# Kernel tuning notes

Hardware: AMD Instinct MI355X
Metric: run time of the kernel (lower is better)

The kernel has to match this reference:

```python
import jax, jax.numpy as jnp
import numpy as np

EMBED_DIM = 1024
FFN_DIM = 12  # == n_qubits; MeasureAll output dim must equal ffn_dim
BATCH, SEQ = 8, 2048


def setup_inputs() -> dict:
    key = jax.random.key(0)
    ks = jax.random.split(key, 6)
    s1 = 1.0 / np.sqrt(EMBED_DIM)
    s2 = 1.0 / np.sqrt(FFN_DIM)
    return {
        "x": jax.random.normal(ks[0], (BATCH, SEQ, EMBED_DIM), dtype=jnp.float32),
        "W1": jax.random.normal(ks[1], (FFN_DIM, EMBED_DIM), dtype=jnp.float32) * s1,
        "b1": jax.random.normal(ks[2], (FFN_DIM,), dtype=jnp.float32) * s1,
        "theta": jax.random.normal(ks[3], (FFN_DIM,), dtype=jnp.float32),
        "W2": jax.random.normal(ks[4], (EMBED_DIM, FFN_DIM), dtype=jnp.float32) * s2,
        "b2": jax.random.normal(ks[5], (EMBED_DIM,), dtype=jnp.float32) * s2,
    }


def reference(x, W1, b1, theta, W2, b2):
    # linear1 + ReLU: (B,S,E) -> (B,S,F)
    h = jax.nn.relu(jnp.einsum("bse,fe->bsf", x, W1) + b1)
    # QLayer: each wire i starts in |0>, gets RX(h_i) then RX(theta_i);
    # product state => <Z_i> = cos(h_i + theta_i) exactly (RX = exp(-i*phi*X/2)).
    q = jnp.cos(h + theta)
    # linear2 (dropout is identity in eval mode)
    return jnp.einsum("bsf,ef->bse", q, W2) + b2
```

## Files before the change

### kernel.cpp

```cpp
#include <hip/hip_runtime.h>
#include <hip/hip_bf16.h>

#define E 1024
#define F 12
#define BM 16

typedef float f32x4_t __attribute__((ext_vector_type(4)));
typedef short bf16x8  __attribute__((ext_vector_type(8)));

__device__ __forceinline__ short f2bf(float f) {
    return (short)__builtin_bit_cast(unsigned short, __float2bfloat16(f));
}

__global__ __launch_bounds__(256, 4) void ffq_mfma(
    const float* __restrict__ x,
    const float* __restrict__ W1,
    const float* __restrict__ b1,
    const float* __restrict__ theta,
    const float* __restrict__ W2,
    const float* __restrict__ b2,
    float* __restrict__ out, int nrows)
{
    const int tid  = threadIdx.x;
    const int lane = tid & 63;
    const int wave = tid >> 6;
    const int g    = lane >> 4;
    const int n    = lane & 15;

    const int row0 = blockIdx.x * BM;
    if (row0 >= nrows) return;

    __shared__ __align__(16) float red[4][64][4];
    __shared__ __align__(16) float qsh[16][20];

    float w2l[48];
#pragma unroll
    for (int k2 = 0; k2 < 12; ++k2)
        *reinterpret_cast<f32x4_t*>(&w2l[4 * k2]) =
            *reinterpret_cast<const f32x4_t*>(W2 + (size_t)tid * 48 + 4 * k2);
    const f32x4_t bias2 = *reinterpret_cast<const f32x4_t*>(b2 + tid * 4);

    const int nc = (n < F) ? n : (F - 1);
    const float b1n = b1[nc], thn = theta[nc];

    const int mrow = min(row0 + n, nrows - 1);
    const float* xrow = x  + (size_t)mrow * E + wave * 256 + g * 8;
    const float* wrow = W1 + (size_t)nc   * E + wave * 256 + g * 8;

    f32x4_t acc0 = {0.f, 0.f, 0.f, 0.f}, acc1 = {0.f, 0.f, 0.f, 0.f};
#pragma unroll
    for (int ks = 0; ks < 8; ++ks) {
        f32x4_t a0 = *reinterpret_cast<const f32x4_t*>(xrow + ks * 32);
        f32x4_t a1 = *reinterpret_cast<const f32x4_t*>(xrow + ks * 32 + 4);
        f32x4_t b0 = *reinterpret_cast<const f32x4_t*>(wrow + ks * 32);
        f32x4_t b1v= *reinterpret_cast<const f32x4_t*>(wrow + ks * 32 + 4);
        bf16x8 af, bfr;
#pragma unroll
        for (int j = 0; j < 4; ++j) {
            af[j]      = f2bf(a0[j]);
            af[j + 4]  = f2bf(a1[j]);
            bfr[j]     = f2bf(b0[j]);
            bfr[j + 4] = f2bf(b1v[j]);
        }
        if (ks & 1) acc1 = __builtin_amdgcn_mfma_f32_16x16x32_bf16(af, bfr, acc1, 0, 0, 0);
        else        acc0 = __builtin_amdgcn_mfma_f32_16x16x32_bf16(af, bfr, acc0, 0, 0, 0);
    }
    *reinterpret_cast<f32x4_t*>(&red[wave][lane][0]) = acc0 + acc1;

    __syncthreads();

    {
        f32x4_t r0 = *reinterpret_cast<const f32x4_t*>(&red[0][lane][0]);
        f32x4_t r1 = *reinterpret_cast<const f32x4_t*>(&red[1][lane][0]);
        f32x4_t r2 = *reinterpret_cast<const f32x4_t*>(&red[2][lane][0]);
        f32x4_t r3 = *reinterpret_cast<const f32x4_t*>(&red[3][lane][0]);
        f32x4_t s  = (r0 + r1) + (r2 + r3);
#pragma unroll
        for (int j = 0; j < 4; ++j) {
            const int m = g * 4 + j;
            qsh[m][n] = __cosf(fmaxf(s[j] + b1n, 0.0f) + thn);
        }
    }

    float* orow = out + (size_t)row0 * E + tid * 4;
#pragma unroll 4
    for (int m = 0; m < BM; ++m) {
        if (row0 + m < nrows) {
            float qf[F];
            *reinterpret_cast<f32x4_t*>(&qf[0]) = *reinterpret_cast<const f32x4_t*>(&qsh[m][0]);
            *reinterpret_cast<f32x4_t*>(&qf[4]) = *reinterpret_cast<const f32x4_t*>(&qsh[m][4]);
            *reinterpret_cast<f32x4_t*>(&qf[8]) = *reinterpret_cast<const f32x4_t*>(&qsh[m][8]);

            f32x4_t o;
#pragma unroll
            for (int j = 0; j < 4; ++j) {
                float a = bias2[j];
#pragma unroll
                for (int f = 0; f < F; ++f) a = fmaf(qf[f], w2l[12 * j + f], a);
                o[j] = a;
            }
            *reinterpret_cast<f32x4_t*>(orow + (size_t)m * E) = o;
        }
    }
}

extern "C" void kernel_launch(void* const* d_in, const int* in_sizes, int n_in,
                              void* d_out, int out_size, void* d_ws, size_t ws_size,
                              hipStream_t stream)
{
    const float* x     = (const float*)d_in[0];
    const float* W1    = (const float*)d_in[1];
    const float* b1    = (const float*)d_in[2];
    const float* theta = (const float*)d_in[3];
    const float* W2    = (const float*)d_in[4];
    const float* b2    = (const float*)d_in[5];
    float* out = (float*)d_out;

    const int nrows = in_sizes[0] / E;
    const int grid  = (nrows + BM - 1) / BM;

    ffq_mfma<<<grid, 256, 0, stream>>>(x, W1, b1, theta, W2, b2, out, nrows);
}
```

Measured before the change: 31.78 us.

## Collapse block to a single wave computing full K reduction, drop LDS reduce

Each block is now one 64-thread wave that runs all 32 K-steps of the bf16 MFMA itself. This removes the cross-wave shared-memory reduction and the __syncthreads. The output stage loops over four 256-column chunks, reloading W2 slices per chunk, and writes with nontemporal stores. The trade-off is far fewer resident waves per CU with the same grid, which reduces memory-level parallelism in a bandwidth-bound kernel.

Result: slower. 34.69 us (+9.2%).

```diff
diff --git a/kernel.cpp b/kernel.cpp
--- a/kernel.cpp
+++ b/kernel.cpp
@@ -12,7 +12,7 @@
     return (short)__builtin_bit_cast(unsigned short, __float2bfloat16(f));
 }
 
-__global__ __launch_bounds__(256, 4) void ffq_mfma(
+__global__ __launch_bounds__(64, 2) void ffq_wave(
     const float* __restrict__ x,
     const float* __restrict__ W1,
     const float* __restrict__ b1,
@@ -21,39 +21,29 @@
     const float* __restrict__ b2,
     float* __restrict__ out, int nrows)
 {
-    const int tid  = threadIdx.x;
-    const int lane = tid & 63;
-    const int wave = tid >> 6;
+    const int lane = threadIdx.x & 63;
     const int g    = lane >> 4;
     const int n    = lane & 15;
 
     const int row0 = blockIdx.x * BM;
     if (row0 >= nrows) return;
 
-    __shared__ __align__(16) float red[4][64][4];
     __shared__ __align__(16) float qsh[16][20];
-
-    float w2l[48];
-#pragma unroll
-    for (int k2 = 0; k2 < 12; ++k2)
-        *reinterpret_cast<f32x4_t*>(&w2l[4 * k2]) =
-            *reinterpret_cast<const f32x4_t*>(W2 + (size_t)tid * 48 + 4 * k2);
-    const f32x4_t bias2 = *reinterpret_cast<const f32x4_t*>(b2 + tid * 4);
 
     const int nc = (n < F) ? n : (F - 1);
     const float b1n = b1[nc], thn = theta[nc];
 
     const int mrow = min(row0 + n, nrows - 1);
-    const float* xrow = x  + (size_t)mrow * E + wave * 256 + g * 8;
-    const float* wrow = W1 + (size_t)nc   * E + wave * 256 + g * 8;
+    const float* xrow = x  + (size_t)mrow * E + g * 8;
+    const float* wrow = W1 + (size_t)nc   * E + g * 8;
 
     f32x4_t acc0 = {0.f, 0.f, 0.f, 0.f}, acc1 = {0.f, 0.f, 0.f, 0.f};
 #pragma unroll
-    for (int ks = 0; ks < 8; ++ks) {
-        f32x4_t a0 = *reinterpret_cast<const f32x4_t*>(xrow + ks * 32);
-        f32x4_t a1 = *reinterpret_cast<const f32x4_t*>(xrow + ks * 32 + 4);
-        f32x4_t b0 = *reinterpret_cast<const f32x4_t*>(wrow + ks * 32);
-        f32x4_t b1v= *reinterpret_cast<const f32x4_t*>(wrow + ks * 32 + 4);
+    for (int kb = 0; kb < 32; ++kb) {
+        f32x4_t a0 = *reinterpret_cast<const f32x4_t*>(xrow + kb * 32);
+        f32x4_t a1 = *reinterpret_cast<const f32x4_t*>(xrow + kb * 32 + 4);
+        f32x4_t b0 = *reinterpret_cast<const f32x4_t*>(wrow + kb * 32);
+        f32x4_t b1v= *reinterpret_cast<const f32x4_t*>(wrow + kb * 32 + 4);
         bf16x8 af, bfr;
 #pragma unroll
         for (int j = 0; j < 4; ++j) {
@@ -62,44 +52,47 @@
             bfr[j]     = f2bf(b0[j]);
             bfr[j + 4] = f2bf(b1v[j]);
         }
-        if (ks & 1) acc1 = __builtin_amdgcn_mfma_f32_16x16x32_bf16(af, bfr, acc1, 0, 0, 0);
+        if (kb & 1) acc1 = __builtin_amdgcn_mfma_f32_16x16x32_bf16(af, bfr, acc1, 0, 0, 0);
         else        acc0 = __builtin_amdgcn_mfma_f32_16x16x32_bf16(af, bfr, acc0, 0, 0, 0);
     }
-    *reinterpret_cast<f32x4_t*>(&red[wave][lane][0]) = acc0 + acc1;
-
-    __syncthreads();
 
     {
-        f32x4_t r0 = *reinterpret_cast<const f32x4_t*>(&red[0][lane][0]);
-        f32x4_t r1 = *reinterpret_cast<const f32x4_t*>(&red[1][lane][0]);
-        f32x4_t r2 = *reinterpret_cast<const f32x4_t*>(&red[2][lane][0]);
-        f32x4_t r3 = *reinterpret_cast<const f32x4_t*>(&red[3][lane][0]);
-        f32x4_t s  = (r0 + r1) + (r2 + r3);
+        f32x4_t s = acc0 + acc1;
 #pragma unroll
-        for (int j = 0; j < 4; ++j) {
-            const int m = g * 4 + j;
-            qsh[m][n] = __cosf(fmaxf(s[j] + b1n, 0.0f) + thn);
-        }
+        for (int j = 0; j < 4; ++j)
+            qsh[g * 4 + j][n] = __cosf(fmaxf(s[j] + b1n, 0.0f) + thn);
     }
 
-    float* orow = out + (size_t)row0 * E + tid * 4;
+#pragma unroll
+    for (int c = 0; c < 4; ++c) {
+        const int e0 = c * 256 + lane * 4;
+
+        float w2l[48];
+#pragma unroll
+        for (int k2 = 0; k2 < 12; ++k2)
+            *reinterpret_cast<f32x4_t*>(&w2l[4 * k2]) =
+                *reinterpret_cast<const f32x4_t*>(W2 + (size_t)e0 * F + 4 * k2);
+        const f32x4_t bias2 = *reinterpret_cast<const f32x4_t*>(b2 + e0);
+
 #pragma unroll 4
-    for (int m = 0; m < BM; ++m) {
-        if (row0 + m < nrows) {
-            float qf[F];
-            *reinterpret_cast<f32x4_t*>(&qf[0]) = *reinterpret_cast<const f32x4_t*>(&qsh[m][0]);
-            *reinterpret_cast<f32x4_t*>(&qf[4]) = *reinterpret_cast<const f32x4_t*>(&qsh[m][4]);
-            *reinterpret_cast<f32x4_t*>(&qf[8]) = *reinterpret_cast<const f32x4_t*>(&qsh[m][8]);
+        for (int m = 0; m < BM; ++m) {
+            if (row0 + m < nrows) {
+                float qf[F];
+                *reinterpret_cast<f32x4_t*>(&qf[0]) = *reinterpret_cast<const f32x4_t*>(&qsh[m][0]);
+                *reinterpret_cast<f32x4_t*>(&qf[4]) = *reinterpret_cast<const f32x4_t*>(&qsh[m][4]);
+                *reinterpret_cast<f32x4_t*>(&qf[8]) = *reinterpret_cast<const f32x4_t*>(&qsh[m][8]);
 
-            f32x4_t o;
+                f32x4_t o;
 #pragma unroll
-            for (int j = 0; j < 4; ++j) {
-                float a = bias2[j];
+                for (int j = 0; j < 4; ++j) {
+                    float a = bias2[j];
 #pragma unroll
-                for (int f = 0; f < F; ++f) a = fmaf(qf[f], w2l[12 * j + f], a);
-                o[j] = a;
+                    for (int f = 0; f < F; ++f) a = fmaf(qf[f], w2l[12 * j + f], a);
+                    o[j] = a;
+                }
+                __builtin_nontemporal_store(o,
+                    reinterpret_cast<f32x4_t*>(out + (size_t)(row0 + m) * E + e0));
             }
-            *reinterpret_cast<f32x4_t*>(orow + (size_t)m * E) = o;
         }
     }
 }
@@ -119,5 +112,5 @@
     const int nrows = in_sizes[0] / E;
     const int grid  = (nrows + BM - 1) / BM;
 
-    ffq_mfma<<<grid, 256, 0, stream>>>(x, W1, b1, theta, W2, b2, out, nrows);
+    ffq_wave<<<grid, 64, 0, stream>>>(x, W1, b1, theta, W2, b2, out, nrows);
 }
```
